# Performance work log

Measured on AMD Instinct MI355X. Metric: run time of the kernel, lower is better.

## Reference

```python
import jax, jax.numpy as jnp
import numpy as np

N_NODES = 50000
N_EDGES = 800000
IN, HID, OUT = 128, [128, 128], 64


def setup_inputs() -> dict:
    key = jax.random.key(0)
    ks = jax.random.split(key, 10)
    inp = {
        'in_feat': jax.random.normal(ks[0], (N_NODES, IN), dtype=jnp.float32),
        'src': jax.random.randint(ks[1], (N_EDGES,), 0, N_NODES, dtype=jnp.int32),
        'dst': jax.random.randint(ks[2], (N_EDGES,), 0, N_NODES, dtype=jnp.int32),
    }
    dims = [IN] + HID + [OUT]  # [128,128,128,64]
    for i in range(3):
        fan_in = dims[i]
        inp[f'W{i}'] = jax.random.normal(ks[3 + i], (dims[i + 1], dims[i]), dtype=jnp.float32) / np.sqrt(fan_in)
        inp[f'b{i}'] = jnp.zeros((dims[i + 1],), dtype=jnp.float32)
    return inp


def _sage_gcn_layer(x, W, b, src, dst, n_nodes):
    # DGL SAGEConv aggregator_type='gcn':
    #   neigh = segment_sum of src feats over dst edges (graph already has self-loops)
    #   h = (neigh + x) / (in_degree + 1); out = h @ W.T + b
    msg = x[src]                                             # [E, d] gather
    neigh = jax.ops.segment_sum(msg, dst, num_segments=n_nodes)
    deg = jax.ops.segment_sum(jnp.ones(src.shape[0], x.dtype), dst, num_segments=n_nodes)
    h = (neigh + x) / (deg[:, None] + 1.0)
    return h @ W.T + b


def reference(in_feat, src, dst, W0, b0, W1, b1, W2, b2):
    n = in_feat.shape[0]
    # remove_self_loop + add_self_loop -> exactly one self loop per node
    loop = jnp.arange(n, dtype=src.dtype)
    src_f = jnp.concatenate([src, loop])
    dst_f = jnp.concatenate([dst, loop])
    # Dropout(0.5) is identity in eval mode.
    h = in_feat
    h = jax.nn.relu(_sage_gcn_layer(h, W0, b0, src_f, dst_f, n))
    h = jax.nn.relu(_sage_gcn_layer(h, W1, b1, src_f, dst_f, n))
    h = _sage_gcn_layer(h, W2, b2, src_f, dst_f, n)
    return h
```

## Files before the change

kernel.cpp:

```cpp
#include <hip/hip_runtime.h>
#include <hip/hip_bf16.h>


#define NFEAT 128
#define BKT_CAP 12288
#define CHUNK 64

using bf16x8 = __attribute__((ext_vector_type(8))) short;
using f32x4  = __attribute__((ext_vector_type(4))) float;

__device__ __forceinline__ ushort f2bf(float f) {
    unsigned u = __float_as_uint(f);
    u = (u + 0x7fffu + ((u >> 16) & 1u)) >> 16;
    return (ushort)u;
}
__device__ __forceinline__ float bflo(unsigned v) { return __uint_as_float(v << 16); }
__device__ __forceinline__ float bfhi(unsigned v) { return __uint_as_float(v & 0xffff0000u); }

__device__ __forceinline__ int xcc_id() {
    int x;
    asm volatile("s_getreg_b32 %0, hwreg(HW_REG_XCC_ID)" : "=s"(x));
    return x & 7;
}


__global__ __launch_bounds__(256) void k_init(unsigned* __restrict__ esrc_u32, int fillN, unsigned sent2,
                                              int* __restrict__ ctl, ushort* __restrict__ Ybuf, int n,
                                              const float* __restrict__ W0, const float* __restrict__ W1,
                                              const float* __restrict__ W2, ushort* __restrict__ Wb) {
    int i = blockIdx.x * 256 + threadIdx.x;
    if (i < fillN) {
        esrc_u32[i] = sent2;
    } else if (i < fillN + 336) {
        ctl[i - fillN] = 0;
    } else if (i < fillN + 336 + 64) {
        int j = i - fillN - 336;
        int p = j >> 4, k = j & 15;
        ((unsigned*)(Ybuf + (size_t)p * (n + 1) * 32 + (size_t)n * 32))[k] = 0u;
    } else if (i < fillN + 336 + 64 + 40960) {
        int j = i - fillN - 336 - 64;
        float v = (j < 16384) ? W0[j] : ((j < 32768) ? W1[j - 16384] : W2[j - 32768]);
        Wb[j] = f2bf(v);
    }
}


__global__ __launch_bounds__(256) void k_bin(const int* __restrict__ src, const int* __restrict__ dst,
                                             int* __restrict__ gcur, unsigned* __restrict__ pairs, int ne) {
    __shared__ int lcnt[128];
    __shared__ int lbase[128];
    int tid = threadIdx.x;
    if (tid < 128) lcnt[tid] = 0;
    __syncthreads();
    int e0 = blockIdx.x * 4096;
    int myrank[16];
    int mybkt[16];
    unsigned mypair[16];
    #pragma unroll
    for (int blk = 0; blk < 4; ++blk) {
        int e = e0 + blk * 1024 + tid * 4;
        int4 s4, d4;
        bool full = (e + 3 < ne);
        if (full) {
            s4 = *(const int4*)&src[e];
            d4 = *(const int4*)&dst[e];
        } else {
            s4.x = (e + 0 < ne) ? src[e + 0] : 0;  d4.x = (e + 0 < ne) ? dst[e + 0] : -1;
            s4.y = (e + 1 < ne) ? src[e + 1] : 0;  d4.y = (e + 1 < ne) ? dst[e + 1] : -1;
            s4.z = (e + 2 < ne) ? src[e + 2] : 0;  d4.z = (e + 2 < ne) ? dst[e + 2] : -1;
            s4.w = (e + 3 < ne) ? src[e + 3] : 0;  d4.w = (e + 3 < ne) ? dst[e + 3] : -1;
        }
        int ss[4] = {s4.x, s4.y, s4.z, s4.w};
        int dd[4] = {d4.x, d4.y, d4.z, d4.w};
        #pragma unroll
        for (int c = 0; c < 4; ++c) {
            int i = blk * 4 + c;
            if (dd[c] >= 0) {
                int b = dd[c] >> 9;
                mybkt[i]  = b;
                mypair[i] = (unsigned)(ss[c] & 0xffff) | ((unsigned)(dd[c] & 511) << 16);
                myrank[i] = atomicAdd(&lcnt[b], 1);
            } else mybkt[i] = -1;
        }
    }
    __syncthreads();
    if (tid < 128) lbase[tid] = lcnt[tid] ? atomicAdd(&gcur[tid], lcnt[tid]) : 0;
    __syncthreads();
    #pragma unroll
    for (int i = 0; i < 16; ++i) {
        if (mybkt[i] >= 0) {
            int pos = lbase[mybkt[i]] + myrank[i];
            if (pos < BKT_CAP) pairs[(size_t)mybkt[i] * BKT_CAP + pos] = mypair[i];
        }
    }
}


__global__ __launch_bounds__(1024) void k_cntprep(const unsigned* __restrict__ pairs, const int* __restrict__ gcur,
                                                  int* __restrict__ cnt, int* __restrict__ perm,
                                                  int* __restrict__ offs, int* __restrict__ gbase,
                                                  ushort* __restrict__ esrc, int n) {
    __shared__ int lcnt[1024];
    __shared__ int loffs[1024];
    __shared__ int hist[256];
    __shared__ int hcur[256];
    __shared__ int wtot[16];
    __shared__ int wpre[16];
    __shared__ int sbase;
    int tid  = threadIdx.x;
    int lane = tid & 63;
    int wv   = tid >> 6;
    int base = blockIdx.x * 1024;
    lcnt[tid] = 0;
    if (tid < 256) hist[tid] = 0;
    __syncthreads();
    #pragma unroll
    for (int h = 0; h < 2; ++h) {
        int bkt = blockIdx.x * 2 + h;
        int m = gcur[bkt];
        if (m > BKT_CAP) m = BKT_CAP;
        const unsigned* p = pairs + (size_t)bkt * BKT_CAP;
        for (int i = tid; i < m; i += 1024)
            atomicAdd(&lcnt[(int)(p[i] >> 16) + h * 512], 1);
    }
    __syncthreads();
    int i   = base + tid;
    bool act = i < n;
    int c = act ? lcnt[tid] : 0;
    if (act) cnt[i] = c;
    int d = c > 255 ? 255 : c;
    int rank = 0;
    if (act) rank = atomicAdd(&hist[d], 1);
    __syncthreads();
    {
        int v = (tid < 256) ? hist[tid] : 0;
        int val = v;
        #pragma unroll
        for (int off = 1; off < 64; off <<= 1) {
            int t = __shfl_up(val, off);
            if (lane >= off) val += t;
        }
        if (lane == 63) wtot[wv] = val;
        __syncthreads();
        if (tid == 0) {
            int s = 0;
            #pragma unroll
            for (int w = 0; w < 4; ++w) { wpre[w] = s; s += wtot[w]; }
        }
        __syncthreads();
        if (tid < 256) hcur[tid] = val - v + wpre[wv];
        __syncthreads();
        if (act) perm[base + hcur[d] + rank] = i;
        __syncthreads();
    }
    {
        int p8 = act ? ((c + 7) & ~7) : 0;
        int val = p8;
        #pragma unroll
        for (int off = 1; off < 64; off <<= 1) {
            int t = __shfl_up(val, off);
            if (lane >= off) val += t;
        }
        if (lane == 63) wtot[wv] = val;
        __syncthreads();
        if (tid == 0) {
            int s = 0;
            #pragma unroll
            for (int w = 0; w < 16; ++w) { wpre[w] = s; s += wtot[w]; }
            sbase = atomicAdd(gbase, s);
        }
        __syncthreads();
        int myoff = sbase + val - p8 + wpre[wv];
        if (act) offs[i] = myoff;
        loffs[tid] = myoff;
        lcnt[tid]  = 0;
    }
    __syncthreads();
    #pragma unroll
    for (int h = 0; h < 2; ++h) {
        int bkt = blockIdx.x * 2 + h;
        int m = gcur[bkt];
        if (m > BKT_CAP) m = BKT_CAP;
        const unsigned* p = pairs + (size_t)bkt * BKT_CAP;
        for (int j = tid; j < m; j += 1024) {
            unsigned pr = p[j];
            int w = (int)(pr >> 16) + h * 512;
            int r = atomicAdd(&lcnt[w], 1);
            esrc[loffs[w] + r] = (ushort)(pr & 0xffffu);
        }
    }
}


template <typename InT, int N, bool PLANES_IN>
__global__ __launch_bounds__(256) void k_gemm_mfma(const InT* __restrict__ X, const ushort* __restrict__ Wb,
                                                   ushort* __restrict__ Y, int M, int Mp) {
    int w    = threadIdx.x >> 6;
    int lane = threadIdx.x & 63;
    int kb   = (lane >> 4) * 8;
    int rbase = blockIdx.x * 128 + w * 16 + (lane & 15);

    bf16x8 a0[4], a1[4];
    #pragma unroll
    for (int set = 0; set < 2; ++set) {
        int rowf = rbase + set * 64;
        bf16x8* a = set ? a1 : a0;
        if (rowf < M) {
            #pragma unroll
            for (int ks = 0; ks < 4; ++ks) {
                if constexpr (PLANES_IN) {
                    a[ks] = *(const bf16x8*)((const ushort*)X + (size_t)ks * Mp * 32 + (size_t)rowf * 32 + kb);
                } else {
                    const float* xp = (const float*)X + (size_t)rowf * 128 + ks * 32 + kb;
                    float4 f0 = *(const float4*)xp;
                    float4 f1 = *(const float4*)(xp + 4);
                    bf16x8 t;
                    t[0] = f2bf(f0.x); t[1] = f2bf(f0.y); t[2] = f2bf(f0.z); t[3] = f2bf(f0.w);
                    t[4] = f2bf(f1.x); t[5] = f2bf(f1.y); t[6] = f2bf(f1.z); t[7] = f2bf(f1.w);
                    a[ks] = t;
                }
            }
        } else {
            #pragma unroll
            for (int ks = 0; ks < 4; ++ks) {
                bf16x8 z = {0, 0, 0, 0, 0, 0, 0, 0};
                a[ks] = z;
            }
        }
    }

    constexpr int NT = N / 16;
    int c  = lane & 15;
    int rr = blockIdx.x * 128 + w * 16 + (lane >> 4) * 4;
    #pragma unroll
    for (int nt = 0; nt < NT; ++nt) {
        f32x4 acc0 = (f32x4){0.f, 0.f, 0.f, 0.f};
        f32x4 acc1 = (f32x4){0.f, 0.f, 0.f, 0.f};
        const ushort* wp = Wb + (size_t)(nt * 16 + (lane & 15)) * 128 + kb;
        #pragma unroll
        for (int ks = 0; ks < 4; ++ks) {
            bf16x8 b = *(const bf16x8*)(wp + ks * 32);
            acc0 = __builtin_amdgcn_mfma_f32_16x16x32_bf16(a0[ks], b, acc0, 0, 0, 0);
            acc1 = __builtin_amdgcn_mfma_f32_16x16x32_bf16(a1[ks], b, acc1, 0, 0, 0);
        }
        size_t pl = (size_t)(nt >> 1) * Mp * 32 + (nt & 1) * 16 + c;
        #pragma unroll
        for (int j = 0; j < 4; ++j) {
            int r = rr + j;
            if (r < M) Y[pl + (size_t)r * 32] = (ushort)f2bf(acc0[j]);
        }
        #pragma unroll
        for (int j = 0; j < 4; ++j) {
            int r = rr + 64 + j;
            if (r < M) Y[pl + (size_t)r * 32] = (ushort)f2bf(acc1[j]);
        }
    }
}


#define ACC8(T)  { a0 += bflo((T).x); a1 += bfhi((T).x); a2 += bflo((T).y); a3 += bfhi((T).y); \
                   a4 += bflo((T).z); a5 += bfhi((T).z); a6 += bflo((T).w); a7 += bfhi((T).w); }

template <bool RELU>
__global__ __launch_bounds__(256) void k_agg128(const ushort* __restrict__ Yp, const int* __restrict__ offs,
                                                const int* __restrict__ cnt, const ushort* __restrict__ esrc,
                                                const float* __restrict__ bias, ushort* __restrict__ Zp,
                                                const int* __restrict__ perm, int* __restrict__ qh,
                                                int n, int nchunk) {
    __shared__ int sQ, sT;
    if (threadIdx.x == 0) {
        int pref = xcc_id() & 3;
        int t = -1, qsel = 0;
        #pragma unroll
        for (int a = 0; a < 4; ++a) {
            int cand = (pref + a) & 3;
            int tt = atomicAdd(&qh[cand * 16], 1);
            if (tt < nchunk) { qsel = cand; t = tt; break; }
        }
        sQ = qsel; sT = t;
    }
    __syncthreads();
    int q = sQ, t = sT;
    if (t < 0) return;
    int lane = threadIdx.x & 63;
    int wv   = threadIdx.x >> 6;
    int g    = lane >> 2;
    int sub  = lane & 3;
    int idx  = t * CHUNK + wv * 16 + g;
    bool active = idx < n;
    int nd = 0, start = 0, deg = 0;
    if (active) {
        nd    = perm[idx];
        start = offs[nd];
        deg   = cnt[nd];
    }
    const uint4* Y4 = (const uint4*)(Yp + (size_t)q * (n + 1) * 32);
    uint4*       Z4 = (uint4*)(Zp + (size_t)q * (n + 1) * 32);

    float a0 = 0.f, a1 = 0.f, a2 = 0.f, a3 = 0.f, a4 = 0.f, a5 = 0.f, a6 = 0.f, a7 = 0.f;

    int nblk = active ? ((deg + 7) >> 3) : 0;
    const uint4* ep = (const uint4*)(esrc + start);
    uint4 ib = ep[0];
    #pragma unroll 2
    for (int b = 0; b < nblk; ++b) {
        uint4 ibn = ep[b + 1];
        unsigned s0 = ib.x & 0xffffu, s1 = ib.x >> 16;
        unsigned s2 = ib.y & 0xffffu, s3 = ib.y >> 16;
        unsigned s4 = ib.z & 0xffffu, s5 = ib.z >> 16;
        unsigned s6 = ib.w & 0xffffu, s7 = ib.w >> 16;
        uint4 t0 = Y4[(size_t)s0 * 4 + sub];
        uint4 t1 = Y4[(size_t)s1 * 4 + sub];
        uint4 t2 = Y4[(size_t)s2 * 4 + sub];
        uint4 t3 = Y4[(size_t)s3 * 4 + sub];
        uint4 t4 = Y4[(size_t)s4 * 4 + sub];
        uint4 t5 = Y4[(size_t)s5 * 4 + sub];
        uint4 t6 = Y4[(size_t)s6 * 4 + sub];
        uint4 t7 = Y4[(size_t)s7 * 4 + sub];
        ACC8(t0); ACC8(t1); ACC8(t2); ACC8(t3); ACC8(t4); ACC8(t5); ACC8(t6); ACC8(t7);
        ib = ibn;
    }

    if (active) {
        float scale = 1.0f / (float)(deg + 2);
        uint4 sf = Y4[(size_t)nd * 4 + sub];
        int f0 = q * 32 + sub * 8;
        float4 bA = *(const float4*)&bias[f0];
        float4 bB = *(const float4*)&bias[f0 + 4];
        float r0 = (a0 + 2.f * bflo(sf.x)) * scale + bA.x;
        float r1 = (a1 + 2.f * bfhi(sf.x)) * scale + bA.y;
        float r2 = (a2 + 2.f * bflo(sf.y)) * scale + bA.z;
        float r3 = (a3 + 2.f * bfhi(sf.y)) * scale + bA.w;
        float r4 = (a4 + 2.f * bflo(sf.z)) * scale + bB.x;
        float r5 = (a5 + 2.f * bfhi(sf.z)) * scale + bB.y;
        float r6 = (a6 + 2.f * bflo(sf.w)) * scale + bB.z;
        float r7 = (a7 + 2.f * bfhi(sf.w)) * scale + bB.w;
        if (RELU) {
            r0 = fmaxf(r0, 0.f); r1 = fmaxf(r1, 0.f); r2 = fmaxf(r2, 0.f); r3 = fmaxf(r3, 0.f);
            r4 = fmaxf(r4, 0.f); r5 = fmaxf(r5, 0.f); r6 = fmaxf(r6, 0.f); r7 = fmaxf(r7, 0.f);
        }
        uint4 o;
        o.x = (unsigned)f2bf(r0) | ((unsigned)f2bf(r1) << 16);
        o.y = (unsigned)f2bf(r2) | ((unsigned)f2bf(r3) << 16);
        o.z = (unsigned)f2bf(r4) | ((unsigned)f2bf(r5) << 16);
        o.w = (unsigned)f2bf(r6) | ((unsigned)f2bf(r7) << 16);
        Z4[(size_t)nd * 4 + sub] = o;
    }
}

__global__ __launch_bounds__(256) void k_agg64(const ushort* __restrict__ Yp, const int* __restrict__ offs,
                                               const int* __restrict__ cnt, const ushort* __restrict__ esrc,
                                               const float* __restrict__ bias, float* __restrict__ Z,
                                               const int* __restrict__ perm, int* __restrict__ qh,
                                               int n, int nchunk) {
    __shared__ int sQ, sT;
    if (threadIdx.x == 0) {
        int pref = xcc_id() & 1;
        int t = -1, qsel = 0;
        #pragma unroll
        for (int a = 0; a < 2; ++a) {
            int cand = (pref + a) & 1;
            int tt = atomicAdd(&qh[cand * 16], 1);
            if (tt < nchunk) { qsel = cand; t = tt; break; }
        }
        sQ = qsel; sT = t;
    }
    __syncthreads();
    int h = sQ, t = sT;
    if (t < 0) return;
    int lane = threadIdx.x & 63;
    int wv   = threadIdx.x >> 6;
    int g    = lane >> 2;
    int sub  = lane & 3;
    int idx  = t * CHUNK + wv * 16 + g;
    bool active = idx < n;
    int nd = 0, start = 0, deg = 0;
    if (active) {
        nd    = perm[idx];
        start = offs[nd];
        deg   = cnt[nd];
    }
    const uint4* Y4 = (const uint4*)(Yp + (size_t)h * (n + 1) * 32);

    float a0 = 0.f, a1 = 0.f, a2 = 0.f, a3 = 0.f, a4 = 0.f, a5 = 0.f, a6 = 0.f, a7 = 0.f;

    int nblk = active ? ((deg + 7) >> 3) : 0;
    const uint4* ep = (const uint4*)(esrc + start);
    uint4 ib = ep[0];
    #pragma unroll 2
    for (int b = 0; b < nblk; ++b) {
        uint4 ibn = ep[b + 1];
        unsigned s0 = ib.x & 0xffffu, s1 = ib.x >> 16;
        unsigned s2 = ib.y & 0xffffu, s3 = ib.y >> 16;
        unsigned s4 = ib.z & 0xffffu, s5 = ib.z >> 16;
        unsigned s6 = ib.w & 0xffffu, s7 = ib.w >> 16;
        uint4 t0 = Y4[(size_t)s0 * 4 + sub];
        uint4 t1 = Y4[(size_t)s1 * 4 + sub];
        uint4 t2 = Y4[(size_t)s2 * 4 + sub];
        uint4 t3 = Y4[(size_t)s3 * 4 + sub];
        uint4 t4 = Y4[(size_t)s4 * 4 + sub];
        uint4 t5 = Y4[(size_t)s5 * 4 + sub];
        uint4 t6 = Y4[(size_t)s6 * 4 + sub];
        uint4 t7 = Y4[(size_t)s7 * 4 + sub];
        ACC8(t0); ACC8(t1); ACC8(t2); ACC8(t3); ACC8(t4); ACC8(t5); ACC8(t6); ACC8(t7);
        ib = ibn;
    }

    if (active) {
        float scale = 1.0f / (float)(deg + 2);
        uint4 sf = Y4[(size_t)nd * 4 + sub];
        int f0 = h * 32 + sub * 8;
        float4 bA = *(const float4*)&bias[f0];
        float4 bB = *(const float4*)&bias[f0 + 4];
        float4 oA, oB;
        oA.x = (a0 + 2.f * bflo(sf.x)) * scale + bA.x;
        oA.y = (a1 + 2.f * bfhi(sf.x)) * scale + bA.y;
        oA.z = (a2 + 2.f * bflo(sf.y)) * scale + bA.z;
        oA.w = (a3 + 2.f * bfhi(sf.y)) * scale + bA.w;
        oB.x = (a4 + 2.f * bflo(sf.z)) * scale + bB.x;
        oB.y = (a5 + 2.f * bfhi(sf.z)) * scale + bB.y;
        oB.z = (a6 + 2.f * bflo(sf.w)) * scale + bB.z;
        oB.w = (a7 + 2.f * bfhi(sf.w)) * scale + bB.w;
        float* zr = Z + (size_t)nd * 64 + f0;
        *(float4*)zr       = oA;
        *(float4*)(zr + 4) = oB;
    }
}


extern "C" void kernel_launch(void* const* d_in, const int* in_sizes, int n_in,
                              void* d_out, int out_size, void* d_ws, size_t ws_size,
                              hipStream_t stream) {
    const float* in_feat = (const float*)d_in[0];
    const int*   src     = (const int*)d_in[1];
    const int*   dst     = (const int*)d_in[2];
    const float* W0      = (const float*)d_in[3];
    const float* b0      = (const float*)d_in[4];
    const float* W1      = (const float*)d_in[5];
    const float* b1      = (const float*)d_in[6];
    const float* W2      = (const float*)d_in[7];
    const float* b2      = (const float*)d_in[8];
    float* out = (float*)d_out;

    const int n  = in_sizes[0] / NFEAT;
    const int ne = in_sizes[1];
    const int nch = (n + 1023) / 1024;
    const int nchunk = (n + CHUNK - 1) / CHUNK;
    const int escap = (ne + 8 * n + 31) & ~15;

    int* offs       = (int*)d_ws;
    int* gcur       = offs + ((n + 4) & ~3);
    int* qh         = gcur + 128;
    int* gbase      = qh + 192;
    int* cnt        = gbase + 16;
    int* perm       = cnt + ((n + 3) & ~3);
    unsigned* pairs = (unsigned*)(perm + ((n + 3) & ~3));
    ushort* esrc    = (ushort*)(pairs + (size_t)128 * BKT_CAP);
    ushort* Wb      = esrc + escap;
    ushort* Ybuf    = Wb + 40960;
    ushort* Zbuf    = Ybuf + (size_t)(n + 1) * NFEAT;

    const int fillN = escap / 2;
    const unsigned sent2 = ((unsigned)n << 16) | (unsigned)n;
    const int initN = fillN + 336 + 64 + 40960;
    k_init<<<(initN + 255) / 256, 256, 0, stream>>>((unsigned*)esrc, fillN, sent2, gcur, Ybuf, n,
                                                    W0, W1, W2, Wb);

    k_bin<<<(ne + 4095) / 4096, 256, 0, stream>>>(src, dst, gcur, pairs, ne);
    k_cntprep<<<nch, 1024, 0, stream>>>(pairs, gcur, cnt, perm, offs, gbase, esrc, n);

    const ushort* Wb0 = Wb;
    const ushort* Wb1 = Wb + 16384;
    const ushort* Wb2 = Wb + 32768;

    const int gg = (n + 127) / 128;
    const int Mp = n + 1;

    k_gemm_mfma<float, 128, false><<<gg, 256, 0, stream>>>(in_feat, Wb0, Ybuf, n, Mp);
    k_agg128<true><<<4 * nchunk, 256, 0, stream>>>(Ybuf, offs, cnt, esrc, b0, Zbuf, perm, qh, n, nchunk);
    k_gemm_mfma<ushort, 128, true><<<gg, 256, 0, stream>>>(Zbuf, Wb1, Ybuf, n, Mp);
    k_agg128<true><<<4 * nchunk, 256, 0, stream>>>(Ybuf, offs, cnt, esrc, b1, Zbuf, perm, qh + 64, n, nchunk);
    k_gemm_mfma<ushort, 64, true><<<gg, 256, 0, stream>>>(Zbuf, Wb2, Ybuf, n, Mp);
    k_agg64<<<2 * nchunk, 256, 0, stream>>>(Ybuf, offs, cnt, esrc, b2, out, perm, qh + 128, n, nchunk);

    (void)ws_size; (void)n_in; (void)out_size;
}
```

Baseline: 189.7 us.

## Pad edge lists in cntprep instead of prefilling, add nontemporal loads/stores

Drops the full sentinel fill of the esrc buffer in k_init. Only the padding slots of each node's 8-aligned edge list are now written with the sentinel, at the end of k_cntprep. Streaming loads and stores in the GEMM and aggregation kernels become nontemporal, so they pollute the cache less and leave room for the randomly gathered feature rows. The risk is that nontemporal hints on data reused by the next kernel could hurt it, and the per-thread padding loop is serial.

```diff
diff --git a/kernel.cpp b/kernel.cpp
--- a/kernel.cpp
+++ b/kernel.cpp
@@ -8,6 +8,7 @@
 
 using bf16x8 = __attribute__((ext_vector_type(8))) short;
 using f32x4  = __attribute__((ext_vector_type(4))) float;
+using u32x4  = __attribute__((ext_vector_type(4))) unsigned;
 
 __device__ __forceinline__ ushort f2bf(float f) {
     unsigned u = __float_as_uint(f);
@@ -24,21 +25,18 @@
 }
 
 
-__global__ __launch_bounds__(256) void k_init(unsigned* __restrict__ esrc_u32, int fillN, unsigned sent2,
-                                              int* __restrict__ ctl, ushort* __restrict__ Ybuf, int n,
+__global__ __launch_bounds__(256) void k_init(int* __restrict__ ctl, ushort* __restrict__ Ybuf, int n,
                                               const float* __restrict__ W0, const float* __restrict__ W1,
                                               const float* __restrict__ W2, ushort* __restrict__ Wb) {
     int i = blockIdx.x * 256 + threadIdx.x;
-    if (i < fillN) {
-        esrc_u32[i] = sent2;
-    } else if (i < fillN + 336) {
-        ctl[i - fillN] = 0;
-    } else if (i < fillN + 336 + 64) {
-        int j = i - fillN - 336;
+    if (i < 336) {
+        ctl[i] = 0;
+    } else if (i < 336 + 64) {
+        int j = i - 336;
         int p = j >> 4, k = j & 15;
         ((unsigned*)(Ybuf + (size_t)p * (n + 1) * 32 + (size_t)n * 32))[k] = 0u;
-    } else if (i < fillN + 336 + 64 + 40960) {
-        int j = i - fillN - 336 - 64;
+    } else if (i < 336 + 64 + 40960) {
+        int j = i - 336 - 64;
         float v = (j < 16384) ? W0[j] : ((j < 32768) ? W1[j - 16384] : W2[j - 32768]);
         Wb[j] = f2bf(v);
     }
@@ -153,8 +151,9 @@
         if (act) perm[base + hcur[d] + rank] = i;
         __syncthreads();
     }
+    int p8 = 0, myoff = 0;
     {
-        int p8 = act ? ((c + 7) & ~7) : 0;
+        p8 = act ? ((c + 7) & ~7) : 0;
         int val = p8;
         #pragma unroll
         for (int off = 1; off < 64; off <<= 1) {
@@ -170,7 +169,7 @@
             sbase = atomicAdd(gbase, s);
         }
         __syncthreads();
-        int myoff = sbase + val - p8 + wpre[wv];
+        myoff = sbase + val - p8 + wpre[wv];
         if (act) offs[i] = myoff;
         loffs[tid] = myoff;
         lcnt[tid]  = 0;
@@ -189,6 +188,9 @@
             esrc[loffs[w] + r] = (ushort)(pr & 0xffffu);
         }
     }
+    if (act) {
+        for (int j = c; j < p8; ++j) esrc[myoff + j] = (ushort)n;
+    }
 }
 
 
@@ -209,14 +211,15 @@
             #pragma unroll
             for (int ks = 0; ks < 4; ++ks) {
                 if constexpr (PLANES_IN) {
-                    a[ks] = *(const bf16x8*)((const ushort*)X + (size_t)ks * Mp * 32 + (size_t)rowf * 32 + kb);
+                    a[ks] = __builtin_nontemporal_load(
+                        (const bf16x8*)((const ushort*)X + (size_t)ks * Mp * 32 + (size_t)rowf * 32 + kb));
                 } else {
                     const float* xp = (const float*)X + (size_t)rowf * 128 + ks * 32 + kb;
-                    float4 f0 = *(const float4*)xp;
-                    float4 f1 = *(const float4*)(xp + 4);
+                    f32x4 f0 = __builtin_nontemporal_load((const f32x4*)xp);
+                    f32x4 f1 = __builtin_nontemporal_load((const f32x4*)(xp + 4));
                     bf16x8 t;
-                    t[0] = f2bf(f0.x); t[1] = f2bf(f0.y); t[2] = f2bf(f0.z); t[3] = f2bf(f0.w);
-                    t[4] = f2bf(f1.x); t[5] = f2bf(f1.y); t[6] = f2bf(f1.z); t[7] = f2bf(f1.w);
+                    t[0] = f2bf(f0[0]); t[1] = f2bf(f0[1]); t[2] = f2bf(f0[2]); t[3] = f2bf(f0[3]);
+                    t[4] = f2bf(f1[0]); t[5] = f2bf(f1[1]); t[6] = f2bf(f1[2]); t[7] = f2bf(f1[3]);
                     a[ks] = t;
                 }
             }
@@ -247,19 +250,19 @@
         #pragma unroll
         for (int j = 0; j < 4; ++j) {
             int r = rr + j;
-            if (r < M) Y[pl + (size_t)r * 32] = (ushort)f2bf(acc0[j]);
+            if (r < M) __builtin_nontemporal_store((ushort)f2bf(acc0[j]), &Y[pl + (size_t)r * 32]);
         }
         #pragma unroll
         for (int j = 0; j < 4; ++j) {
             int r = rr + 64 + j;
-            if (r < M) Y[pl + (size_t)r * 32] = (ushort)f2bf(acc1[j]);
-        }
-    }
-}
-
-
-#define ACC8(T)  { a0 += bflo((T).x); a1 += bfhi((T).x); a2 += bflo((T).y); a3 += bfhi((T).y); \
-                   a4 += bflo((T).z); a5 += bfhi((T).z); a6 += bflo((T).w); a7 += bfhi((T).w); }
+            if (r < M) __builtin_nontemporal_store((ushort)f2bf(acc1[j]), &Y[pl + (size_t)r * 32]);
+        }
+    }
+}
+
+
+#define ACC8(T)  { a0 += bflo((T)[0]); a1 += bfhi((T)[0]); a2 += bflo((T)[1]); a3 += bfhi((T)[1]); \
+                   a4 += bflo((T)[2]); a5 += bfhi((T)[2]); a6 += bflo((T)[3]); a7 += bfhi((T)[3]); }
 
 template <bool RELU>
 __global__ __launch_bounds__(256) void k_agg128(const ushort* __restrict__ Yp, const int* __restrict__ offs,
@@ -294,57 +297,57 @@
         start = offs[nd];
         deg   = cnt[nd];
     }
-    const uint4* Y4 = (const uint4*)(Yp + (size_t)q * (n + 1) * 32);
-    uint4*       Z4 = (uint4*)(Zp + (size_t)q * (n + 1) * 32);
+    const u32x4* Y4 = (const u32x4*)(Yp + (size_t)q * (n + 1) * 32);
+    u32x4*       Z4 = (u32x4*)(Zp + (size_t)q * (n + 1) * 32);
 
     float a0 = 0.f, a1 = 0.f, a2 = 0.f, a3 = 0.f, a4 = 0.f, a5 = 0.f, a6 = 0.f, a7 = 0.f;
 
     int nblk = active ? ((deg + 7) >> 3) : 0;
-    const uint4* ep = (const uint4*)(esrc + start);
-    uint4 ib = ep[0];
+    const u32x4* ep = (const u32x4*)(esrc + start);
+    u32x4 ib = __builtin_nontemporal_load(ep);
     #pragma unroll 2
     for (int b = 0; b < nblk; ++b) {
-        uint4 ibn = ep[b + 1];
-        unsigned s0 = ib.x & 0xffffu, s1 = ib.x >> 16;
-        unsigned s2 = ib.y & 0xffffu, s3 = ib.y >> 16;
-        unsigned s4 = ib.z & 0xffffu, s5 = ib.z >> 16;
-        unsigned s6 = ib.w & 0xffffu, s7 = ib.w >> 16;
-        uint4 t0 = Y4[(size_t)s0 * 4 + sub];
-        uint4 t1 = Y4[(size_t)s1 * 4 + sub];
-        uint4 t2 = Y4[(size_t)s2 * 4 + sub];
-        uint4 t3 = Y4[(size_t)s3 * 4 + sub];
-        uint4 t4 = Y4[(size_t)s4 * 4 + sub];
-        uint4 t5 = Y4[(size_t)s5 * 4 + sub];
-        uint4 t6 = Y4[(size_t)s6 * 4 + sub];
-        uint4 t7 = Y4[(size_t)s7 * 4 + sub];
+        u32x4 ibn = __builtin_nontemporal_load(ep + b + 1);
+        unsigned s0 = ib[0] & 0xffffu, s1 = ib[0] >> 16;
+        unsigned s2 = ib[1] & 0xffffu, s3 = ib[1] >> 16;
+        unsigned s4 = ib[2] & 0xffffu, s5 = ib[2] >> 16;
+        unsigned s6 = ib[3] & 0xffffu, s7 = ib[3] >> 16;
+        u32x4 t0 = Y4[(size_t)s0 * 4 + sub];
+        u32x4 t1 = Y4[(size_t)s1 * 4 + sub];
+        u32x4 t2 = Y4[(size_t)s2 * 4 + sub];
+        u32x4 t3 = Y4[(size_t)s3 * 4 + sub];
+        u32x4 t4 = Y4[(size_t)s4 * 4 + sub];
+        u32x4 t5 = Y4[(size_t)s5 * 4 + sub];
+        u32x4 t6 = Y4[(size_t)s6 * 4 + sub];
+        u32x4 t7 = Y4[(size_t)s7 * 4 + sub];
         ACC8(t0); ACC8(t1); ACC8(t2); ACC8(t3); ACC8(t4); ACC8(t5); ACC8(t6); ACC8(t7);
         ib = ibn;
     }
 
     if (active) {
         float scale = 1.0f / (float)(deg + 2);
-        uint4 sf = Y4[(size_t)nd * 4 + sub];
+        u32x4 sf = Y4[(size_t)nd * 4 + sub];
         int f0 = q * 32 + sub * 8;
         float4 bA = *(const float4*)&bias[f0];
         float4 bB = *(const float4*)&bias[f0 + 4];
-        float r0 = (a0 + 2.f * bflo(sf.x)) * scale + bA.x;
-        float r1 = (a1 + 2.f * bfhi(sf.x)) * scale + bA.y;
-        float r2 = (a2 + 2.f * bflo(sf.y)) * scale + bA.z;
-        float r3 = (a3 + 2.f * bfhi(sf.y)) * scale + bA.w;
-        float r4 = (a4 + 2.f * bflo(sf.z)) * scale + bB.x;
-        float r5 = (a5 + 2.f * bfhi(sf.z)) * scale + bB.y;
-        float r6 = (a6 + 2.f * bflo(sf.w)) * scale + bB.z;
-        float r7 = (a7 + 2.f * bfhi(sf.w)) * scale + bB.w;
+        float r0 = (a0 + 2.f * bflo(sf[0])) * scale + bA.x;
+        float r1 = (a1 + 2.f * bfhi(sf[0])) * scale + bA.y;
+        float r2 = (a2 + 2.f * bflo(sf[1])) * scale + bA.z;
+        float r3 = (a3 + 2.f * bfhi(sf[1])) * scale + bA.w;
+        float r4 = (a4 + 2.f * bflo(sf[2])) * scale + bB.x;
+        float r5 = (a5 + 2.f * bfhi(sf[2])) * scale + bB.y;
+        float r6 = (a6 + 2.f * bflo(sf[3])) * scale + bB.z;
+        float r7 = (a7 + 2.f * bfhi(sf[3])) * scale + bB.w;
         if (RELU) {
             r0 = fmaxf(r0, 0.f); r1 = fmaxf(r1, 0.f); r2 = fmaxf(r2, 0.f); r3 = fmaxf(r3, 0.f);
             r4 = fmaxf(r4, 0.f); r5 = fmaxf(r5, 0.f); r6 = fmaxf(r6, 0.f); r7 = fmaxf(r7, 0.f);
         }
-        uint4 o;
-        o.x = (unsigned)f2bf(r0) | ((unsigned)f2bf(r1) << 16);
-        o.y = (unsigned)f2bf(r2) | ((unsigned)f2bf(r3) << 16);
-        o.z = (unsigned)f2bf(r4) | ((unsigned)f2bf(r5) << 16);
-        o.w = (unsigned)f2bf(r6) | ((unsigned)f2bf(r7) << 16);
-        Z4[(size_t)nd * 4 + sub] = o;
+        u32x4 o;
+        o[0] = (unsigned)f2bf(r0) | ((unsigned)f2bf(r1) << 16);
+        o[1] = (unsigned)f2bf(r2) | ((unsigned)f2bf(r3) << 16);
+        o[2] = (unsigned)f2bf(r4) | ((unsigned)f2bf(r5) << 16);
+        o[3] = (unsigned)f2bf(r6) | ((unsigned)f2bf(r7) << 16);
+        __builtin_nontemporal_store(o, Z4 + (size_t)nd * 4 + sub);
     }
 }
 
@@ -380,50 +383,50 @@
         start = offs[nd];
         deg   = cnt[nd];
     }
-    const uint4* Y4 = (const uint4*)(Yp + (size_t)h * (n + 1) * 32);
+    const u32x4* Y4 = (const u32x4*)(Yp + (size_t)h * (n + 1) * 32);
 
     float a0 = 0.f, a1 = 0.f, a2 = 0.f, a3 = 0.f, a4 = 0.f, a5 = 0.f, a6 = 0.f, a7 = 0.f;
 
     int nblk = active ? ((deg + 7) >> 3) : 0;
-    const uint4* ep = (const uint4*)(esrc + start);
-    uint4 ib = ep[0];
+    const u32x4* ep = (const u32x4*)(esrc + start);
+    u32x4 ib = __builtin_nontemporal_load(ep);
     #pragma unroll 2
     for (int b = 0; b < nblk; ++b) {
-        uint4 ibn = ep[b + 1];
-        unsigned s0 = ib.x & 0xffffu, s1 = ib.x >> 16;
-        unsigned s2 = ib.y & 0xffffu, s3 = ib.y >> 16;
-        unsigned s4 = ib.z & 0xffffu, s5 = ib.z >> 16;
-        unsigned s6 = ib.w & 0xffffu, s7 = ib.w >> 16;
-        uint4 t0 = Y4[(size_t)s0 * 4 + sub];
-        uint4 t1 = Y4[(size_t)s1 * 4 + sub];
-        uint4 t2 = Y4[(size_t)s2 * 4 + sub];
-        uint4 t3 = Y4[(size_t)s3 * 4 + sub];
-        uint4 t4 = Y4[(size_t)s4 * 4 + sub];
-        uint4 t5 = Y4[(size_t)s5 * 4 + sub];
-        uint4 t6 = Y4[(size_t)s6 * 4 + sub];
-        uint4 t7 = Y4[(size_t)s7 * 4 + sub];
+        u32x4 ibn = __builtin_nontemporal_load(ep + b + 1);
+        unsigned s0 = ib[0] & 0xffffu, s1 = ib[0] >> 16;
+        unsigned s2 = ib[1] & 0xffffu, s3 = ib[1] >> 16;
+        unsigned s4 = ib[2] & 0xffffu, s5 = ib[2] >> 16;
+        unsigned s6 = ib[3] & 0xffffu, s7 = ib[3] >> 16;
+        u32x4 t0 = Y4[(size_t)s0 * 4 + sub];
+        u32x4 t1 = Y4[(size_t)s1 * 4 + sub];
+        u32x4 t2 = Y4[(size_t)s2 * 4 + sub];
+        u32x4 t3 = Y4[(size_t)s3 * 4 + sub];
+        u32x4 t4 = Y4[(size_t)s4 * 4 + sub];
+        u32x4 t5 = Y4[(size_t)s5 * 4 + sub];
+        u32x4 t6 = Y4[(size_t)s6 * 4 + sub];
+        u32x4 t7 = Y4[(size_t)s7 * 4 + sub];
         ACC8(t0); ACC8(t1); ACC8(t2); ACC8(t3); ACC8(t4); ACC8(t5); ACC8(t6); ACC8(t7);
         ib = ibn;
     }
 
     if (active) {
         float scale = 1.0f / (float)(deg + 2);
-        uint4 sf = Y4[(size_t)nd * 4 + sub];
+        u32x4 sf = Y4[(size_t)nd * 4 + sub];
         int f0 = h * 32 + sub * 8;
         float4 bA = *(const float4*)&bias[f0];
         float4 bB = *(const float4*)&bias[f0 + 4];
-        float4 oA, oB;
-        oA.x = (a0 + 2.f * bflo(sf.x)) * scale + bA.x;
-        oA.y = (a1 + 2.f * bfhi(sf.x)) * scale + bA.y;
-        oA.z = (a2 + 2.f * bflo(sf.y)) * scale + bA.z;
-        oA.w = (a3 + 2.f * bfhi(sf.y)) * scale + bA.w;
-        oB.x = (a4 + 2.f * bflo(sf.z)) * scale + bB.x;
-        oB.y = (a5 + 2.f * bfhi(sf.z)) * scale + bB.y;
-        oB.z = (a6 + 2.f * bflo(sf.w)) * scale + bB.z;
-        oB.w = (a7 + 2.f * bfhi(sf.w)) * scale + bB.w;
+        f32x4 oA, oB;
+        oA[0] = (a0 + 2.f * bflo(sf[0])) * scale + bA.x;
+        oA[1] = (a1 + 2.f * bfhi(sf[0])) * scale + bA.y;
+        oA[2] = (a2 + 2.f * bflo(sf[1])) * scale + bA.z;
+        oA[3] = (a3 + 2.f * bfhi(sf[1])) * scale + bA.w;
+        oB[0] = (a4 + 2.f * bflo(sf[2])) * scale + bB.x;
+        oB[1] = (a5 + 2.f * bfhi(sf[2])) * scale + bB.y;
+        oB[2] = (a6 + 2.f * bflo(sf[3])) * scale + bB.z;
+        oB[3] = (a7 + 2.f * bfhi(sf[3])) * scale + bB.w;
         float* zr = Z + (size_t)nd * 64 + f0;
-        *(float4*)zr       = oA;
-        *(float4*)(zr + 4) = oB;
+        __builtin_nontemporal_store(oA, (f32x4*)zr);
+        __builtin_nontemporal_store(oB, (f32x4*)(zr + 4));
     }
 }
 
@@ -460,11 +463,8 @@
     ushort* Ybuf    = Wb + 40960;
     ushort* Zbuf    = Ybuf + (size_t)(n + 1) * NFEAT;
 
-    const int fillN = escap / 2;
-    const unsigned sent2 = ((unsigned)n << 16) | (unsigned)n;
-    const int initN = fillN + 336 + 64 + 40960;
-    k_init<<<(initN + 255) / 256, 256, 0, stream>>>((unsigned*)esrc, fillN, sent2, gcur, Ybuf, n,
-                                                    W0, W1, W2, Wb);
+    const int initN = 336 + 64 + 40960;
+    k_init<<<(initN + 255) / 256, 256, 0, stream>>>(gcur, Ybuf, n, W0, W1, W2, Wb);
 
     k_bin<<<(ne + 4095) / 4096, 256, 0, stream>>>(src, dst, gcur, pairs, ne);
     k_cntprep<<<nch, 1024, 0, stream>>>(pairs, gcur, cnt, perm, offs, gbase, esrc, n);
```

Result: slower. 205.8 us (+8.5%).
